# Optimization experiments

Measured on AMD Instinct MI355X. Metric: run time of the kernel, lower is better.

The kernel has to match this reference:

```python
import jax, jax.numpy as jnp
import numpy as np

B, N, D, H, NDIMS, NS = 4, 1024, 512, 8, 3, 1
HD = D // H


def setup_inputs() -> dict:
    key = jax.random.key(0)
    ks = jax.random.split(key, 10)
    x = jax.random.normal(ks[0], (B, N, D), dtype=jnp.float32)
    coords = jax.random.normal(ks[1], (B, N, NDIMS), dtype=jnp.float32)
    # pad last 64 key positions in half the batch
    key_padding_mask = jnp.zeros((B, N), dtype=bool).at[: B // 2, -64:].set(True)
    s = 1.0 / np.sqrt(D)
    Wqkv = jax.random.normal(ks[2], (3 * D, D), dtype=jnp.float32) * s  # torch Linear weight [out,in]
    Wout = jax.random.normal(ks[3], (D, D), dtype=jnp.float32) * s
    bout = jnp.zeros((D,), dtype=jnp.float32)
    fin = NDIMS + 1  # num_dims>1 -> dist channel appended
    W1 = jax.random.normal(ks[4], (H * 4, fin), dtype=jnp.float32) / np.sqrt(fin)
    b1 = jnp.zeros((H * 4,), dtype=jnp.float32)
    W2 = jax.random.normal(ks[5], (H, H * 4), dtype=jnp.float32) / np.sqrt(H * 4)
    b2 = jnp.zeros((H,), dtype=jnp.float32)
    bias_alpha = jax.random.normal(ks[6], (1,), dtype=jnp.float32)
    return dict(x=x, coords=coords, key_padding_mask=key_padding_mask,
                bias_alpha=bias_alpha, W1=W1, b1=b1, W2=W2, b2=b2,
                Wqkv=Wqkv, Wout=Wout, bout=bout)


def reference(x, coords, key_padding_mask, bias_alpha, W1, b1, W2, b2, Wqkv, Wout, bout):
    scale = HD ** (-0.5)
    qkv = x @ Wqkv.T  # [B,N,3D]
    q, k, v = jnp.split(qkv, 3, axis=-1)
    q = q.reshape(B, N, H, HD).transpose(0, 2, 1, 3)  # [B,H,N,HD]
    k = k.reshape(B, N, H, HD).transpose(0, 2, 1, 3)
    v = v.reshape(B, N, H, HD).transpose(0, 2, 1, 3)

    dpos = coords[:, :, None, :] - coords[:, None, :, :]  # [B,N,N,ndims]
    dist = jnp.linalg.norm(dpos, axis=-1, keepdims=True)
    dpos = jnp.concatenate([dpos, dist], axis=-1)  # [B,N,N,ndims+1]
    h = jax.nn.gelu(dpos @ W1.T + b1, approximate=False)
    bias = (h @ W2.T + b2).transpose(0, 3, 1, 2)  # [B,H,N,N]
    # zero bias rows/cols for special tokens
    valid = jnp.arange(N) >= NS
    bias = bias * (valid[:, None] & valid[None, :])[None, None]

    dots = jnp.einsum('bhid,bhjd->bhij', q, k) * scale
    logits = dots + bias_alpha[0] * bias
    logits = jnp.where(key_padding_mask[:, None, None, :], -jnp.inf, logits)
    attn = jax.nn.softmax(logits, axis=-1)
    out = jnp.einsum('bhij,bhjd->bhid', attn, v)
    out = out.transpose(0, 2, 1, 3).reshape(B, N, D)
    return out @ Wout.T + bout, attn
```

## Files before the change

### kernel.cpp

```cpp
#include <hip/hip_runtime.h>
#include <hip/hip_fp16.h>
#include <stdint.h>
#include <math.h>

#define B_  4
#define N_  1024
#define D_  512
#define H_  8
#define HD_ 64

typedef short s16x8 __attribute__((ext_vector_type(8)));
typedef float f32x4 __attribute__((ext_vector_type(4)));
typedef float f32x2 __attribute__((ext_vector_type(2)));
typedef __fp16 f16x2 __attribute__((ext_vector_type(2)));

typedef const __attribute__((address_space(1))) void* gas1p;
typedef __attribute__((address_space(3))) void* las3p;
__device__ __forceinline__ void gload16(const void* g, void* l) {
    __builtin_amdgcn_global_load_lds((gas1p)g, (las3p)l, 16, 0, 0);
}

__device__ __forceinline__ unsigned short f2bf(float f) {
    unsigned u = __float_as_uint(f);
    u += 0x7fffu + ((u >> 16) & 1u);
    return (unsigned short)(u >> 16);
}
__device__ __forceinline__ float bf2f(unsigned short h) {
    return __uint_as_float(((unsigned)h) << 16);
}

__device__ __forceinline__ float fast_gelu(float x) {
    float ax = fabsf(x) * 0.7071067811865476f;
    float t  = __builtin_amdgcn_rcpf(fmaf(0.3275911f, ax, 1.0f));
    float e  = __expf(-ax * ax);
    float poly = t * fmaf(t, fmaf(t, fmaf(t, fmaf(t, 1.061405429f, -1.453152027f),
                                          1.421413741f), -0.284496736f), 0.254829592f);
    float erfv = 1.0f - poly * e;
    float s = copysignf(erfv, x);
    return 0.5f * x * (1.0f + s);
}

__global__ void k_split(const float* __restrict__ s, unsigned short* __restrict__ h,
                        unsigned short* __restrict__ l, int n) {
    int i = blockIdx.x * 256 + threadIdx.x;
    if (i < n) {
        float x = s[i];
        unsigned short hb = f2bf(x);
        h[i] = hb;
        l[i] = f2bf(x - bf2f(hb));
    }
}

__global__ void k_mask_detect(const unsigned char* __restrict__ m, int* __restrict__ flag) {
    __shared__ int s;
    if (threadIdx.x == 0) s = 0;
    __syncthreads();
    int found = 0;
    for (int i = threadIdx.x; i < B_ * N_; i += 256)
        if ((i & 3) && m[i]) found = 1;
    if (found) atomicOr(&s, 1);
    __syncthreads();
    if (threadIdx.x == 0) flag[0] = s;
}

__global__ __launch_bounds__(256) void k_gemm3(
    const unsigned short* __restrict__ Ah, const unsigned short* __restrict__ Al,
    const unsigned short* __restrict__ Bwh, const unsigned short* __restrict__ Bwl,
    float* __restrict__ C, const float* __restrict__ bias, int M, int Nn, int K)
{
    constexpr int BM = 64, BN = 128, BK = 64;
    __shared__ unsigned short At[BM * BK];
    __shared__ unsigned short Bt[BN * BK];
    const int tid = threadIdx.x, lane = tid & 63, wid = tid >> 6;
    const int m0 = blockIdx.x * BM, n0 = blockIdx.y * BN;
    const int wm = wid >> 1, wn = wid & 1;
    f32x4 acc[2][4] = {};
    const unsigned short* Aps[3] = {Ah, Ah, Al};
    const unsigned short* Bps[3] = {Bwh, Bwl, Bwh};

    for (int combo = 0; combo < 3; ++combo) {
        const unsigned short* __restrict__ Ap = Aps[combo];
        const unsigned short* __restrict__ Bp = Bps[combo];
        for (int k0 = 0; k0 < K; k0 += BK) {
            __syncthreads();
            #pragma unroll
            for (int r = 0; r < 2; ++r) {
                int s = r * 256 + tid, row = s >> 3, c8 = s & 7;
                gload16(Ap + (size_t)(m0 + row) * K + k0 + c8 * 8, At + s * 8);
            }
            #pragma unroll
            for (int r = 0; r < 4; ++r) {
                int s = r * 256 + tid, row = s >> 3, c8 = s & 7;
                gload16(Bp + (size_t)(n0 + row) * K + k0 + c8 * 8, Bt + s * 8);
            }
            __syncthreads();
            #pragma unroll
            for (int kk = 0; kk < BK; kk += 32) {
                s16x8 a[2], bb[4];
                #pragma unroll
                for (int fm = 0; fm < 2; ++fm)
                    a[fm] = *(const s16x8*)(At + (wm * 32 + fm * 16 + (lane & 15)) * BK + kk + (lane >> 4) * 8);
                #pragma unroll
                for (int fn = 0; fn < 4; ++fn)
                    bb[fn] = *(const s16x8*)(Bt + (wn * 64 + fn * 16 + (lane & 15)) * BK + kk + (lane >> 4) * 8);
                #pragma unroll
                for (int fm = 0; fm < 2; ++fm)
                    #pragma unroll
                    for (int fn = 0; fn < 4; ++fn)
                        acc[fm][fn] = __builtin_amdgcn_mfma_f32_16x16x32_bf16(a[fm], bb[fn], acc[fm][fn], 0, 0, 0);
            }
        }
    }
    #pragma unroll
    for (int fm = 0; fm < 2; ++fm)
        #pragma unroll
        for (int fn = 0; fn < 4; ++fn)
            #pragma unroll
            for (int r = 0; r < 4; ++r) {
                int row  = m0 + wm * 32 + fm * 16 + (lane >> 4) * 4 + r;
                int coln = n0 + wn * 64 + fn * 16 + (lane & 15);
                float v = acc[fm][fn][r];
                if (bias) v += bias[coln];
                C[(size_t)row * Nn + coln] = v;
            }
}

__global__ void k_rearrange(const float* __restrict__ qkv, unsigned short* __restrict__ qp,
                            unsigned short* __restrict__ kp) {
    int t = blockIdx.x * 256 + threadIdx.x;
    int d = t & 63, n = (t >> 6) & 1023, h = (t >> 16) & 7, b = t >> 19;
    const float* src = qkv + ((size_t)(b * N_ + n)) * (3 * D_) + h * HD_ + d;
    float q = src[0], k = src[D_];
    unsigned short qh = f2bf(q), ql = f2bf(q - bf2f(qh));
    unsigned short kh = f2bf(k), kl = f2bf(k - bf2f(kh));
    size_t base = ((size_t)(b * H_ + h) * N_ + n) * 128;
    qp[base + d] = qh; qp[base + 64 + d] = ql;
    kp[base + d] = kh; kp[base + 64 + d] = kl;
}

__global__ void k_vtrans(const float* __restrict__ qkv, unsigned short* __restrict__ vT) {
    __shared__ unsigned short T[64][65];
    int n0 = blockIdx.x * 64, h = blockIdx.y, b = blockIdx.z;
    int tid = threadIdx.x;
    #pragma unroll
    for (int rep = 0; rep < 16; ++rep) {
        int idx = rep * 256 + tid;
        int nl = idx >> 6, d = idx & 63;
        T[nl][d] = f2bf(qkv[((size_t)(b * N_ + n0 + nl)) * (3 * D_) + 2 * D_ + h * HD_ + d]);
    }
    __syncthreads();
    #pragma unroll
    for (int rep = 0; rep < 16; ++rep) {
        int idx = rep * 256 + tid;
        int dl = idx >> 6, nl = idx & 63;
        vT[((size_t)(b * H_ + h) * HD_ + dl) * N_ + n0 + nl] = T[nl][dl];
    }
}

__global__ void k_nodeproj(const float* __restrict__ coords, const float* __restrict__ W1,
                           unsigned short* __restrict__ Pt) {
    int t = blockIdx.x * 256 + threadIdx.x;
    int bn = t & 4095, c = t >> 12;
    const float* cc = coords + (size_t)bn * 3;
    float v = 32.f * (W1[c * 4] * cc[0] + W1[c * 4 + 1] * cc[1] + W1[c * 4 + 2] * cc[2]);
    __half hv = __float2half(v);
    Pt[t] = *(unsigned short*)&hv;
}

__global__ __launch_bounds__(256) void k_bias(
    const float* __restrict__ coords, const float* __restrict__ alpha,
    const float* __restrict__ W1, const float* __restrict__ b1,
    const float* __restrict__ W2, const float* __restrict__ b2,
    const unsigned short* __restrict__ Pt,
    unsigned short* __restrict__ biasH)
{
    __shared__ unsigned short sPj[32 * 256];
    __shared__ float lut[512];
    __shared__ float SPi[32], swd32[32], sb2f[8];
    __shared__ unsigned short sW2h[8 * 32];
    const int tid = threadIdx.x;
    const int bid = blockIdx.x;
    const int j0 = (bid & 3) * 256;
    const int i  = (bid >> 2) & 1023;
    const int b  = bid >> 12;

    {
        float xk = (tid - 128) * 0.03125f;
        float g0 = fast_gelu(xk);
        float g1 = fast_gelu(xk + 0.03125f);
        lut[tid * 2]     = g0;
        lut[tid * 2 + 1] = g1 - g0;
    }
    if (tid < 32) {
        const float* ci = coords + ((size_t)b * N_ + i) * 3;
        float w0 = W1[tid * 4], w1 = W1[tid * 4 + 1], w2 = W1[tid * 4 + 2], w3 = W1[tid * 4 + 3];
        SPi[tid]   = 32.f * (w0 * ci[0] + w1 * ci[1] + w2 * ci[2] + b1[tid]) + 128.f;
        swd32[tid] = 32.f * w3;
    }
    if (tid < 8) sb2f[tid] = b2[tid];
    {
        __half hv = __float2half(W2[tid]);
        sW2h[tid] = *(unsigned short*)&hv;
    }
    {
        #pragma unroll
        for (int p = 0; p < 4; ++p) {
            int idx = p * 256 + tid;
            int row = idx >> 5, off = (idx & 31) * 8;
            *(s16x8*)(sPj + row * 256 + off) =
                *(const s16x8*)(Pt + (size_t)row * (B_ * N_) + b * N_ + j0 + off);
        }
    }
    __syncthreads();

    const int j = j0 + tid;
    const float* ci = coords + ((size_t)b * N_ + i) * 3;
    const float* cj = coords + ((size_t)b * N_ + j) * 3;
    float dx = ci[0] - cj[0], dy = ci[1] - cj[1], dz = ci[2] - cj[2];
    float dist = sqrtf(dx * dx + dy * dy + dz * dz);

    float acc[8];
    #pragma unroll
    for (int h = 0; h < 8; ++h) acc[h] = 0.f;

    #pragma unroll 1
    for (int g = 0; g < 4; ++g) {
        f16x2 gh[4];
        float gprev = 0.f;
        #pragma unroll
        for (int cc = 0; cc < 8; ++cc) {
            int c = g * 8 + cc;
            unsigned short u = sPj[c * 256 + tid];
            float pj = __half2float(*(const __half*)&u);
            float t  = fmaf(swd32[c], dist, SPi[c] - pj);
            float tc = fminf(fmaxf(t, 0.f), 255.f);
            float fi = floorf(tc);
            int   ii = (int)fi;
            float fr = tc - fi;
            f32x2 vs = *(const f32x2*)(lut + ii * 2);
            float gg = fmaf(fr, vs[1], vs[0]);
            float xb = fmaf(t, 0.03125f, -4.f);
            gg = (t > 254.f) ? xb : gg;
            if (cc & 1) gh[cc >> 1] = __builtin_amdgcn_cvt_pkrtz(gprev, gg);
            else        gprev = gg;
        }
        #pragma unroll
        for (int h = 0; h < 8; ++h) {
            const f16x2* wp = (const f16x2*)(sW2h + h * 32 + g * 8);
            acc[h] = __builtin_amdgcn_fdot2(gh[0], wp[0], acc[h], false);
            acc[h] = __builtin_amdgcn_fdot2(gh[1], wp[1], acc[h], false);
            acc[h] = __builtin_amdgcn_fdot2(gh[2], wp[2], acc[h], false);
            acc[h] = __builtin_amdgcn_fdot2(gh[3], wp[3], acc[h], false);
        }
    }

    float vfac = (i >= 1 && j >= 1) ? alpha[0] : 0.f;
    #pragma unroll
    for (int h = 0; h < 8; ++h) {
        __half hv = __float2half(vfac * (acc[h] + sb2f[h]));
        biasH[(((size_t)(b * H_ + h)) * N_ + i) * N_ + j] = *(unsigned short*)&hv;
    }
}

__global__ __launch_bounds__(256, 4) void k_attn(
    const unsigned short* __restrict__ qp, const unsigned short* __restrict__ kp,
    const unsigned short* __restrict__ vT,
    const unsigned short* __restrict__ biasH,
    float* __restrict__ attnout,
    const unsigned char* __restrict__ mraw, const int* __restrict__ flag,
    unsigned short* __restrict__ avh, unsigned short* __restrict__ avl)
{
    __shared__ s16x8 pool16[2048];
    __shared__ unsigned char smask[N_];
    __shared__ float redm[16][4];
    __shared__ float reds[16][4];
    const int tid = threadIdx.x, lane = tid & 63, wid = tid >> 6;

    int flat = blockIdx.x + 64 * (blockIdx.y + 8 * blockIdx.z);
    int swz  = (flat & 7) * 256 + (flat >> 3);
    const int i0 = (swz & 63) * 16;
    const int h  = (swz >> 6) & 7;
    const int b  = swz >> 9;
    const size_t bh = (size_t)(b * H_ + h);
    const int g = lane >> 4;
    const int cl = lane & 15;

    if (flag[0] != 0) {
        for (int i2 = tid; i2 < N_; i2 += 256) smask[i2] = mraw[b * N_ + i2];
    } else {
        const int* mi = (const int*)mraw;
        for (int i2 = tid; i2 < N_; i2 += 256) smask[i2] = (unsigned char)(mi[b * N_ + i2] != 0);
    }

    const unsigned short* qrow = qp + (bh * N_ + i0 + cl) * 128 + g * 8;
    s16x8 aqh0 = *(const s16x8*)(qrow);
    s16x8 aqh1 = *(const s16x8*)(qrow + 32);
    s16x8 aql0 = *(const s16x8*)(qrow + 64);
    s16x8 aql1 = *(const s16x8*)(qrow + 96);

    int soff[4];
    #pragma unroll
    for (int p = 0; p < 4; ++p) {
        int o = p * 4096 + tid * 16;
        int row = o >> 8, offl = o & 255;
        soff[p] = row * 128 + ((offl ^ ((row & 7) << 4)) >> 1);
    }
    const unsigned short* kbase = kp + bh * (size_t)N_ * 128;

    const int lr = wid * 16 + cl;
    int rdoff[4];
    #pragma unroll
    for (int f = 0; f < 4; ++f)
        rdoff[f] = lr * 256 + ((g * 16 + f * 64) ^ ((lr & 7) << 4));

    char* poolb = (char*)pool16;

    #pragma unroll
    for (int p = 0; p < 4; ++p)
        gload16(kbase + soff[p], poolb + p * 4096 + tid * 16);
    __syncthreads();

    f32x4 acc[16];
    #pragma unroll
    for (int c = 0; c < 16; ++c) {
        if (c < 15) {
            const unsigned short* cb = kbase + (size_t)(c + 1) * 8192;
            char* wb = poolb + ((c + 1) & 1) * 16384;
            #pragma unroll
            for (int p = 0; p < 4; ++p)
                gload16(cb + soff[p], wb + p * 4096 + tid * 16);
        }
        char* kb = poolb + (c & 1) * 16384;
        s16x8 k0 = *(const s16x8*)(kb + rdoff[0]);
        s16x8 k1 = *(const s16x8*)(kb + rdoff[1]);
        s16x8 k2 = *(const s16x8*)(kb + rdoff[2]);
        s16x8 k3 = *(const s16x8*)(kb + rdoff[3]);
        f32x4 a = {0.f, 0.f, 0.f, 0.f};
        a = __builtin_amdgcn_mfma_f32_16x16x32_bf16(aqh0, k0, a, 0, 0, 0);
        a = __builtin_amdgcn_mfma_f32_16x16x32_bf16(aqh1, k1, a, 0, 0, 0);
        a = __builtin_amdgcn_mfma_f32_16x16x32_bf16(aqh0, k2, a, 0, 0, 0);
        a = __builtin_amdgcn_mfma_f32_16x16x32_bf16(aqh1, k3, a, 0, 0, 0);
        a = __builtin_amdgcn_mfma_f32_16x16x32_bf16(aql0, k0, a, 0, 0, 0);
        a = __builtin_amdgcn_mfma_f32_16x16x32_bf16(aql1, k1, a, 0, 0, 0);
        acc[c] = a;
        __syncthreads();
    }

    {
        const unsigned short* bsrc = biasH + (bh * N_ + i0) * N_;
        unsigned short* bl = (unsigned short*)poolb;
        #pragma unroll
        for (int p2 = 0; p2 < 8; ++p2) {
            int idx = p2 * 256 + tid;
            gload16(bsrc + (size_t)idx * 8, bl + idx * 8);
        }
    }
    __syncthreads();

    const float scale = 0.125f;
    const unsigned short* bl = (const unsigned short*)poolb;
    #pragma unroll
    for (int j = 0; j < 16; ++j) {
        const int col = (j * 4 + wid) * 16 + cl;
        const bool mj = (smask[col] != 0);
        #pragma unroll
        for (int r = 0; r < 4; ++r) {
            unsigned short u = bl[(g * 4 + r) * 1024 + col];
            float bv = __half2float(*(const __half*)&u);
            acc[j][r] = mj ? -1e30f : fmaf(acc[j][r], scale, bv);
        }
    }

    float m[4];
    #pragma unroll
    for (int r = 0; r < 4; ++r) {
        float mm = acc[0][r];
        #pragma unroll
        for (int j = 1; j < 16; ++j) mm = fmaxf(mm, acc[j][r]);
        m[r] = mm;
    }
    #pragma unroll
    for (int msk = 1; msk < 16; msk <<= 1)
        #pragma unroll
        for (int r = 0; r < 4; ++r) m[r] = fmaxf(m[r], __shfl_xor(m[r], msk));
    if (cl == 0)
        #pragma unroll
        for (int r = 0; r < 4; ++r) redm[g * 4 + r][wid] = m[r];
    __syncthreads();
    #pragma unroll
    for (int r = 0; r < 4; ++r) {
        int row = g * 4 + r;
        m[r] = fmaxf(fmaxf(redm[row][0], redm[row][1]), fmaxf(redm[row][2], redm[row][3]));
    }

    float s[4] = {0.f, 0.f, 0.f, 0.f};
    #pragma unroll
    for (int j = 0; j < 16; ++j)
        #pragma unroll
        for (int r = 0; r < 4; ++r) {
            float e = __expf(acc[j][r] - m[r]);
            acc[j][r] = e;
            s[r] += e;
        }
    #pragma unroll
    for (int msk = 1; msk < 16; msk <<= 1)
        #pragma unroll
        for (int r = 0; r < 4; ++r) s[r] += __shfl_xor(s[r], msk);
    if (cl == 0)
        #pragma unroll
        for (int r = 0; r < 4; ++r) reds[g * 4 + r][wid] = s[r];
    __syncthreads();
    float sinv[4];
    #pragma unroll
    for (int r = 0; r < 4; ++r) {
        int row = g * 4 + r;
        sinv[r] = 1.0f / (reds[row][0] + reds[row][1] + reds[row][2] + reds[row][3]);
    }

    float* gattn = attnout + (bh * N_ + i0) * N_;
    char* Pb = poolb;
    #pragma unroll
    for (int j = 0; j < 16; ++j) {
        const int col = (j * 4 + wid) * 16 + cl;
        #pragma unroll
        for (int r = 0; r < 4; ++r) {
            const int row = g * 4 + r;
            float e = acc[j][r];
            __builtin_nontemporal_store(e * sinv[r], &gattn[(size_t)row * N_ + col]);
            int byte = row * 2048 + ((col * 2) ^ ((row & 7) << 4));
            *(unsigned short*)(Pb + byte) = f2bf(e);
        }
    }
    __syncthreads();

    {
        const int d0 = wid * 16;
        f32x4 acc2 = {0.f, 0.f, 0.f, 0.f};
        const unsigned short* vrow = vT + (bh * HD_ + d0 + cl) * N_ + g * 8;
        const int rowA = cl;
        const int swzb = (rowA & 7) << 4;
        for (int kk = 0; kk < N_; kk += 32) {
            s16x8 bfrag = *(const s16x8*)(vrow + kk);
            int byte = rowA * 2048 + (((kk + g * 8) * 2) ^ swzb);
            s16x8 af = *(const s16x8*)(Pb + byte);
            acc2 = __builtin_amdgcn_mfma_f32_16x16x32_bf16(af, bfrag, acc2, 0, 0, 0);
        }
        #pragma unroll
        for (int r = 0; r < 4; ++r) {
            const int row = g * 4 + r;
            const int dd = d0 + cl;
            float v = acc2[r] * sinv[r];
            unsigned short hv = f2bf(v);
            size_t o = ((size_t)(b * N_) + i0 + row) * D_ + h * HD_ + dd;
            avh[o] = hv;
            avl[o] = f2bf(v - bf2f(hv));
        }
    }
}

extern "C" void kernel_launch(void* const* d_in, const int* in_sizes, int n_in,
                              void* d_out, int out_size, void* d_ws, size_t ws_size,
                              hipStream_t stream) {
    (void)in_sizes; (void)n_in; (void)out_size; (void)ws_size;
    const float* x      = (const float*)d_in[0];
    const float* coords = (const float*)d_in[1];
    const unsigned char* kpm = (const unsigned char*)d_in[2];
    const float* alpha  = (const float*)d_in[3];
    const float* W1     = (const float*)d_in[4];
    const float* b1     = (const float*)d_in[5];
    const float* W2     = (const float*)d_in[6];
    const float* b2     = (const float*)d_in[7];
    const float* Wqkv   = (const float*)d_in[8];
    const float* Wout   = (const float*)d_in[9];
    const float* bout   = (const float*)d_in[10];

    float* out  = (float*)d_out;
    float* attn = out + (size_t)B_ * N_ * D_;

    char* w = (char*)d_ws;
    auto alloc = [&](size_t bytes) { char* p = w; w += (bytes + 255) & ~(size_t)255; return p; };
    const size_t SZ_X  = (size_t)B_ * N_ * D_;
    const size_t SZ_WQ = (size_t)3 * D_ * D_;
    const size_t SZ_WO = (size_t)D_ * D_;

    unsigned short* wo_hi = (unsigned short*)alloc(SZ_WO * 2);
    unsigned short* wo_lo = (unsigned short*)alloc(SZ_WO * 2);
    unsigned short* qp = (unsigned short*)alloc((size_t)B_ * H_ * N_ * 128 * 2);
    unsigned short* kp = (unsigned short*)alloc((size_t)B_ * H_ * N_ * 128 * 2);
    unsigned short* vT = (unsigned short*)alloc((size_t)B_ * H_ * HD_ * N_ * 2);
    unsigned short* av_hi = (unsigned short*)alloc(SZ_X * 2);
    unsigned short* av_lo = (unsigned short*)alloc(SZ_X * 2);
    unsigned short* Pt = (unsigned short*)alloc((size_t)32 * B_ * N_ * 2);
    int* flag = (int*)alloc(256);

    char* uni = (char*)alloc(0);
    unsigned short* x_hi = (unsigned short*)uni;
    unsigned short* x_lo = x_hi + SZ_X;
    unsigned short* wq_hi = x_lo + SZ_X;
    unsigned short* wq_lo = wq_hi + SZ_WQ;
    float* qkv = (float*)(wq_lo + SZ_WQ);
    unsigned short* biasH = (unsigned short*)uni;

    k_split<<<(int)((SZ_X + 255) / 256), 256, 0, stream>>>(x, x_hi, x_lo, (int)SZ_X);
    k_split<<<(int)((SZ_WQ + 255) / 256), 256, 0, stream>>>(Wqkv, wq_hi, wq_lo, (int)SZ_WQ);
    k_split<<<(int)((SZ_WO + 255) / 256), 256, 0, stream>>>(Wout, wo_hi, wo_lo, (int)SZ_WO);
    k_mask_detect<<<1, 256, 0, stream>>>(kpm, flag);
    k_nodeproj<<<(32 * B_ * N_) / 256, 256, 0, stream>>>(coords, W1, Pt);
    k_gemm3<<<dim3(64, 12), 256, 0, stream>>>(x_hi, x_lo, wq_hi, wq_lo, qkv, nullptr,
                                              B_ * N_, 3 * D_, D_);
    k_rearrange<<<(B_ * H_ * N_ * HD_) / 256, 256, 0, stream>>>(qkv, qp, kp);
    k_vtrans<<<dim3(16, H_, B_), 256, 0, stream>>>(qkv, vT);
    k_bias<<<(B_ * N_ * N_) / 256, 256, 0, stream>>>(coords, alpha, W1, b1, W2, b2, Pt, biasH);
    k_attn<<<dim3(64, H_, B_), 256, 0, stream>>>(qp, kp, vT, biasH, attn, kpm, flag, av_hi, av_lo);
    k_gemm3<<<dim3(64, 4), 256, 0, stream>>>(av_hi, av_lo, wo_hi, wo_lo, out, bout,
                                             B_ * N_, D_, D_);
}
```

Before: 237.6 us.

## Use MFMA for bias MLP second layer with node-major projection layout

The per-pair hidden-to-head projection in the bias kernel now runs as a 16x16x32 fp16 MFMA instead of per-thread fdot2 loops. Each wave packs 16 pairs by 32 hidden channels into the A operand and uses W2, padded to 16 heads with zeros, as the B operand. The node projection table is transposed to node-major layout with padded LDS rows so each lane loads its 8 channels with one vector read. Outputs are written as packed 4-element fp16 stores, but half the MFMA columns are wasted on padding heads and the biasH stores become less coalesced.

```diff
diff --git a/kernel.cpp b/kernel.cpp
--- a/kernel.cpp
+++ b/kernel.cpp
@@ -13,6 +13,7 @@
 typedef float f32x4 __attribute__((ext_vector_type(4)));
 typedef float f32x2 __attribute__((ext_vector_type(2)));
 typedef __fp16 f16x2 __attribute__((ext_vector_type(2)));
+typedef __fp16 f16x8 __attribute__((ext_vector_type(8)));
 
 typedef const __attribute__((address_space(1))) void* gas1p;
 typedef __attribute__((address_space(3))) void* las3p;
@@ -158,27 +159,34 @@
 }
 
 __global__ void k_nodeproj(const float* __restrict__ coords, const float* __restrict__ W1,
-                           unsigned short* __restrict__ Pt) {
-    int t = blockIdx.x * 256 + threadIdx.x;
-    int bn = t & 4095, c = t >> 12;
+                           unsigned short* __restrict__ PtT) {
+    int bn = blockIdx.x * 256 + threadIdx.x;
     const float* cc = coords + (size_t)bn * 3;
-    float v = 32.f * (W1[c * 4] * cc[0] + W1[c * 4 + 1] * cc[1] + W1[c * 4 + 2] * cc[2]);
-    __half hv = __float2half(v);
-    Pt[t] = *(unsigned short*)&hv;
+    float c0 = cc[0], c1 = cc[1], c2 = cc[2];
+    unsigned short outv[32];
+    #pragma unroll
+    for (int c = 0; c < 32; ++c) {
+        float v = 32.f * (W1[c * 4] * c0 + W1[c * 4 + 1] * c1 + W1[c * 4 + 2] * c2);
+        __half hv = __float2half(v);
+        outv[c] = *(unsigned short*)&hv;
+    }
+    #pragma unroll
+    for (int k = 0; k < 4; ++k)
+        *(s16x8*)(PtT + (size_t)bn * 32 + k * 8) = *(const s16x8*)(outv + k * 8);
 }
 
 __global__ __launch_bounds__(256) void k_bias(
     const float* __restrict__ coords, const float* __restrict__ alpha,
     const float* __restrict__ W1, const float* __restrict__ b1,
     const float* __restrict__ W2, const float* __restrict__ b2,
-    const unsigned short* __restrict__ Pt,
+    const unsigned short* __restrict__ PtT,
     unsigned short* __restrict__ biasH)
 {
-    __shared__ unsigned short sPj[32 * 256];
+    __shared__ unsigned short sPj[256 * 40];
     __shared__ float lut[512];
     __shared__ float SPi[32], swd32[32], sb2f[8];
-    __shared__ unsigned short sW2h[8 * 32];
-    const int tid = threadIdx.x;
+    __shared__ float sdist[256];
+    const int tid = threadIdx.x, lane = tid & 63, wid = tid >> 6;
     const int bid = blockIdx.x;
     const int j0 = (bid & 3) * 256;
     const int i  = (bid >> 2) & 1023;
@@ -199,38 +207,46 @@
     }
     if (tid < 8) sb2f[tid] = b2[tid];
     {
-        __half hv = __float2half(W2[tid]);
-        sW2h[tid] = *(unsigned short*)&hv;
+        const unsigned short* src = PtT + ((size_t)(b * N_) + j0) * 32;
+        #pragma unroll
+        for (int k = 0; k < 4; ++k) {
+            int idx = k * 256 + tid;
+            *(s16x8*)(sPj + (idx >> 2) * 40 + (idx & 3) * 8) = *(const s16x8*)(src + idx * 8);
+        }
     }
     {
-        #pragma unroll
-        for (int p = 0; p < 4; ++p) {
-            int idx = p * 256 + tid;
-            int row = idx >> 5, off = (idx & 31) * 8;
-            *(s16x8*)(sPj + row * 256 + off) =
-                *(const s16x8*)(Pt + (size_t)row * (B_ * N_) + b * N_ + j0 + off);
-        }
-    }
-    __syncthreads();
-
-    const int j = j0 + tid;
-    const float* ci = coords + ((size_t)b * N_ + i) * 3;
-    const float* cj = coords + ((size_t)b * N_ + j) * 3;
-    float dx = ci[0] - cj[0], dy = ci[1] - cj[1], dz = ci[2] - cj[2];
-    float dist = sqrtf(dx * dx + dy * dy + dz * dz);
-
-    float acc[8];
-    #pragma unroll
-    for (int h = 0; h < 8; ++h) acc[h] = 0.f;
+        const float* ci = coords + ((size_t)b * N_ + i) * 3;
+        const float* cj = coords + ((size_t)b * N_ + j0 + tid) * 3;
+        float dx = ci[0] - cj[0], dy = ci[1] - cj[1], dz = ci[2] - cj[2];
+        sdist[tid] = sqrtf(dx * dx + dy * dy + dz * dz);
+    }
+    __syncthreads();
+
+    const int hh = lane & 15;
+    const int q  = lane >> 4;
+    const float alph = alpha[0];
+    const float vfi = (i >= 1) ? 1.f : 0.f;
+
+    f16x8 bw;
+    {
+        int hw = hh & 7;
+        #pragma unroll
+        for (int e = 0; e < 8; ++e) {
+            float wv = W2[hw * 32 + q * 8 + e];
+            bw[e] = (hh < 8) ? (__fp16)wv : (__fp16)0.f;
+        }
+    }
 
     #pragma unroll 1
-    for (int g = 0; g < 4; ++g) {
-        f16x2 gh[4];
-        float gprev = 0.f;
-        #pragma unroll
-        for (int cc = 0; cc < 8; ++cc) {
-            int c = g * 8 + cc;
-            unsigned short u = sPj[c * 256 + tid];
+    for (int m = 0; m < 4; ++m) {
+        const int pm = m * 16 + hh;
+        const float dist = sdist[wid * 64 + pm];
+        s16x8 praw = *(const s16x8*)(sPj + (wid * 64 + pm) * 40 + q * 8);
+        f16x8 af;
+        #pragma unroll
+        for (int e = 0; e < 8; ++e) {
+            int c = q * 8 + e;
+            unsigned short u = (unsigned short)praw[e];
             float pj = __half2float(*(const __half*)&u);
             float t  = fmaf(swd32[c], dist, SPi[c] - pj);
             float tc = fminf(fmaxf(t, 0.f), 255.f);
@@ -241,24 +257,24 @@
             float gg = fmaf(fr, vs[1], vs[0]);
             float xb = fmaf(t, 0.03125f, -4.f);
             gg = (t > 254.f) ? xb : gg;
-            if (cc & 1) gh[cc >> 1] = __builtin_amdgcn_cvt_pkrtz(gprev, gg);
-            else        gprev = gg;
-        }
-        #pragma unroll
-        for (int h = 0; h < 8; ++h) {
-            const f16x2* wp = (const f16x2*)(sW2h + h * 32 + g * 8);
-            acc[h] = __builtin_amdgcn_fdot2(gh[0], wp[0], acc[h], false);
-            acc[h] = __builtin_amdgcn_fdot2(gh[1], wp[1], acc[h], false);
-            acc[h] = __builtin_amdgcn_fdot2(gh[2], wp[2], acc[h], false);
-            acc[h] = __builtin_amdgcn_fdot2(gh[3], wp[3], acc[h], false);
-        }
-    }
-
-    float vfac = (i >= 1 && j >= 1) ? alpha[0] : 0.f;
-    #pragma unroll
-    for (int h = 0; h < 8; ++h) {
-        __half hv = __float2half(vfac * (acc[h] + sb2f[h]));
-        biasH[(((size_t)(b * H_ + h)) * N_ + i) * N_ + j] = *(unsigned short*)&hv;
+            af[e] = (__fp16)gg;
+        }
+        f32x4 c4 = {0.f, 0.f, 0.f, 0.f};
+        c4 = __builtin_amdgcn_mfma_f32_16x16x32_f16(af, bw, c4, 0, 0, 0);
+        if (hh < 8) {
+            const int jb = j0 + wid * 64 + m * 16 + q * 4;
+            const float b2h = sb2f[hh];
+            float v0 = ((jb     >= 1) ? alph : 0.f) * vfi * (c4[0] + b2h);
+            float v1 = ((jb + 1 >= 1) ? alph : 0.f) * vfi * (c4[1] + b2h);
+            float v2 = ((jb + 2 >= 1) ? alph : 0.f) * vfi * (c4[2] + b2h);
+            float v3 = ((jb + 3 >= 1) ? alph : 0.f) * vfi * (c4[3] + b2h);
+            __half h0 = __float2half(v0), h1 = __float2half(v1);
+            __half h2 = __float2half(v2), h3 = __float2half(v3);
+            unsigned int lo = (unsigned)*(unsigned short*)&h0 | ((unsigned)*(unsigned short*)&h1 << 16);
+            unsigned int hi = (unsigned)*(unsigned short*)&h2 | ((unsigned)*(unsigned short*)&h3 << 16);
+            unsigned long long pk = (unsigned long long)lo | ((unsigned long long)hi << 32);
+            *(unsigned long long*)(biasH + ((size_t)(b * H_ + hh) * N_ + i) * N_ + jb) = pk;
+        }
     }
 }
 
@@ -490,7 +506,7 @@
     unsigned short* vT = (unsigned short*)alloc((size_t)B_ * H_ * HD_ * N_ * 2);
     unsigned short* av_hi = (unsigned short*)alloc(SZ_X * 2);
     unsigned short* av_lo = (unsigned short*)alloc(SZ_X * 2);
-    unsigned short* Pt = (unsigned short*)alloc((size_t)32 * B_ * N_ * 2);
+    unsigned short* PtT = (unsigned short*)alloc((size_t)B_ * N_ * 32 * 2);
     int* flag = (int*)alloc(256);
 
     char* uni = (char*)alloc(0);
@@ -505,12 +521,12 @@
     k_split<<<(int)((SZ_WQ + 255) / 256), 256, 0, stream>>>(Wqkv, wq_hi, wq_lo, (int)SZ_WQ);
     k_split<<<(int)((SZ_WO + 255) / 256), 256, 0, stream>>>(Wout, wo_hi, wo_lo, (int)SZ_WO);
     k_mask_detect<<<1, 256, 0, stream>>>(kpm, flag);
-    k_nodeproj<<<(32 * B_ * N_) / 256, 256, 0, stream>>>(coords, W1, Pt);
+    k_nodeproj<<<(B_ * N_) / 256, 256, 0, stream>>>(coords, W1, PtT);
     k_gemm3<<<dim3(64, 12), 256, 0, stream>>>(x_hi, x_lo, wq_hi, wq_lo, qkv, nullptr,
                                               B_ * N_, 3 * D_, D_);
     k_rearrange<<<(B_ * H_ * N_ * HD_) / 256, 256, 0, stream>>>(qkv, qp, kp);
     k_vtrans<<<dim3(16, H_, B_), 256, 0, stream>>>(qkv, vT);
-    k_bias<<<(B_ * N_ * N_) / 256, 256, 0, stream>>>(coords, alpha, W1, b1, W2, b2, Pt, biasH);
+    k_bias<<<(B_ * N_ * N_) / 256, 256, 0, stream>>>(coords, alpha, W1, b1, W2, b2, PtT, biasH);
     k_attn<<<dim3(64, H_, B_), 256, 0, stream>>>(qp, kp, vT, biasH, attn, kpm, flag, av_hi, av_lo);
     k_gemm3<<<dim3(64, 4), 256, 0, stream>>>(av_hi, av_lo, wo_hi, wo_lo, out, bout,
                                              B_ * N_, D_, D_);
```

New measurement: 236.0 us, median of 2. About the same (-0.7%).
